# Performance work log

Measured on AMD Instinct MI355X. Metric: run time of the kernel, lower is better.

The kernel has to match this reference:

```python
import jax, jax.numpy as jnp
import numpy as np

MARGIN = 0.5
TIME_GAP = 10
EPS = 1e-8  # torch cosine_similarity eps


def setup_inputs() -> dict:
    key = jax.random.key(0)
    hidden_states = jax.random.normal(key, (16, 4096, 512), dtype=jnp.float32)
    return {"hidden_states": hidden_states}


def _sim_shift(h, n, k):
    # cosine similarity between time t and t+k for all valid t, all batches
    # h: [B, S, D], n: [B, S] precomputed norms -> returns [B, S-k]
    dots = jnp.sum(h[:, :-k] * h[:, k:], axis=-1)
    denom = jnp.maximum(n[:, :-k] * n[:, k:], EPS)
    return dots / denom


def reference(hidden_states):
    h = hidden_states
    B, S, D = h.shape
    n = jnp.sqrt(jnp.sum(h * h, axis=-1))  # [B, S], computed once

    # adjacent: sum_t mean_b(1 - sim(t, t+1)) / (S-1) == overall mean
    adjacent_loss = jnp.mean(1.0 - _sim_shift(h, n, 1))

    # distant: shifts k in [TIME_GAP, 2*TIME_GAP), t in [0, S-k)
    distant_total = jnp.zeros((), dtype=h.dtype)
    count = 0
    for k in range(TIME_GAP, min(S, 2 * TIME_GAP)):
        sim = _sim_shift(h, n, k)  # [B, S-k]
        # original sums mean-over-batch per (t,k) pair
        distant_total = distant_total + jnp.sum(jnp.mean(jax.nn.relu(MARGIN - sim), axis=0))
        count += S - k
    distant_loss = distant_total / count if count > 0 else jnp.zeros((), dtype=h.dtype)

    return adjacent_loss + distant_loss
```

## Files before the change

### kernel.cpp

```cpp
#include <hip/hip_runtime.h>
#include <math.h>

constexpr int B_ = 16;
constexpr int S_ = 4096;
constexpr int D_ = 512;
constexpr float MARGIN = 0.5f;
constexpr float EPS = 1e-8f;

constexpr int T_   = 32;
constexpr int ROWS = T_ + 19;
constexpr int RS   = D_ + 8;
constexpr int NBLK = B_ * (S_ / T_);

typedef __attribute__((ext_vector_type(8))) short short8;
typedef __attribute__((ext_vector_type(4))) float floatx4;

template <int CTRL>
__device__ __forceinline__ float dpp_add(float x) {
    int m = __builtin_amdgcn_update_dpp(0, __float_as_int(x), CTRL, 0xf, 0xf, true);
    return x + __int_as_float(m);
}
__device__ __forceinline__ float wave_sum63(float x) {
    x = dpp_add<0x111>(x);
    x = dpp_add<0x112>(x);
    x = dpp_add<0x114>(x);
    x = dpp_add<0x118>(x);
    x = dpp_add<0x142>(x);
    x = dpp_add<0x143>(x);
    return x;
}

__global__ __launch_bounds__(256) void tcl_partial(const float* __restrict__ h,
                                                   float* __restrict__ ws) {
    __shared__ unsigned short sm[ROWS * RS];
    __shared__ float norms[ROWS];
    __shared__ float bsum[4];

    const int tid = threadIdx.x;
    const int b   = blockIdx.x >> 7;
    const int t0  = (blockIdx.x & 127) * T_;
    const float* base = h + (size_t)b * S_ * D_;

#pragma unroll
    for (int it = 0; it < 26; ++it) {
        const int idx = tid + it * 256;
        if (idx < ROWS * 128) {
            const int r  = idx >> 7;
            const int c4 = idx & 127;
            const int t  = t0 + r;
            float4 v = make_float4(0.f, 0.f, 0.f, 0.f);
            if (t < S_) v = *(const float4*)(base + (size_t)t * D_ + c4 * 4);
            ushort4 u;
            u.x = (unsigned short)(__float_as_uint(v.x) >> 16);
            u.y = (unsigned short)(__float_as_uint(v.y) >> 16);
            u.z = (unsigned short)(__float_as_uint(v.z) >> 16);
            u.w = (unsigned short)(__float_as_uint(v.w) >> 16);
            *(ushort4*)&sm[r * RS + c4 * 4] = u;
        }
    }
    __syncthreads();

    const int lane = tid & 63;
    const int w    = tid >> 6;
    const int m16  = lane & 15;
    const int q    = lane >> 4;

    const int AOFF[8] = {0, 0, 0, 16, 16, 16, 32, 35};
    const int BOFF[8] = {0, 16, 32, 16, 32, 35, 32, 35};
    const int CLO[8]  = {0, 16, 32, 16, 32, 48, 32, 48};
    const int CHI[8]  = {15, 31, 47, 31, 47, 50, 47, 50};
    const int DIAG[8] = {1, 0, 0, 1, 0, 0, 1, 1};
    const int SIMS[8] = {1, 1, 1, 1, 1, 1, 0, 0};

    floatx4 acc[2];
#pragma unroll
    for (int jj = 0; jj < 2; ++jj) {
        const int J = w + jj * 4;
        const unsigned short* pa = &sm[(AOFF[J] + m16) * RS + q * 8];
        const unsigned short* pb = &sm[(BOFF[J] + m16) * RS + q * 8];
        floatx4 c = {0.f, 0.f, 0.f, 0.f};
#pragma unroll
        for (int kk = 0; kk < 16; ++kk) {
            short8 af = *(const short8*)(pa + kk * 32);
            short8 bf = *(const short8*)(pb + kk * 32);
            c = __builtin_amdgcn_mfma_f32_16x16x32_bf16(af, bf, c, 0, 0, 0);
        }
        acc[jj] = c;
    }

#pragma unroll
    for (int jj = 0; jj < 2; ++jj) {
        const int J = w + jj * 4;
        if (DIAG[J]) {
            const int gcol = BOFF[J] + m16;
#pragma unroll
            for (int r = 0; r < 4; ++r) {
                const int grow = AOFF[J] + q * 4 + r;
                if (grow == gcol && gcol >= CLO[J] && gcol <= CHI[J])
                    norms[grow] = sqrtf(acc[jj][r]);
            }
        }
    }
    __syncthreads();

    const float w1 = 1.0f / ((float)B_ * (float)(S_ - 1));
    const float w2 = 1.0f / ((float)B_ * (float)(10 * S_ - 145));
    float local = 0.f;
#pragma unroll
    for (int jj = 0; jj < 2; ++jj) {
        const int J = w + jj * 4;
        if (SIMS[J]) {
            const int gcol = BOFF[J] + m16;
            if (gcol >= CLO[J] && gcol <= CHI[J] && (t0 + gcol) < S_) {
                const float nb = norms[gcol];
#pragma unroll
                for (int r = 0; r < 4; ++r) {
                    const int grow = AOFF[J] + q * 4 + r;
                    const int k = gcol - grow;
                    if (k == 1 || (k >= 10 && k <= 19)) {
                        const float na  = norms[grow];
                        const float sim = acc[jj][r] / fmaxf(na * nb, EPS);
                        local += (k == 1) ? w1 * (1.0f - sim)
                                          : w2 * fmaxf(MARGIN - sim, 0.f);
                    }
                }
            }
        }
    }

    local = wave_sum63(local);
    if (lane == 63) bsum[w] = local;
    __syncthreads();
    if (tid == 0) ws[blockIdx.x] = bsum[0] + bsum[1] + bsum[2] + bsum[3];
}

__global__ __launch_bounds__(1024) void tcl_final(const float* __restrict__ ws,
                                                  float* __restrict__ out) {
    float v = 0.f;
    for (int j = threadIdx.x; j < NBLK; j += 1024) v += ws[j];
    v = wave_sum63(v);
    __shared__ float s[16];
    if ((threadIdx.x & 63) == 63) s[threadIdx.x >> 6] = v;
    __syncthreads();
    if (threadIdx.x == 0) {
        float t = 0.f;
#pragma unroll
        for (int j = 0; j < 16; j++) t += s[j];
        out[0] = t;
    }
}

extern "C" void kernel_launch(void* const* d_in, const int* in_sizes, int n_in,
                              void* d_out, int out_size, void* d_ws, size_t ws_size,
                              hipStream_t stream) {
    const float* h = (const float*)d_in[0];
    float* out = (float*)d_out;
    float* ws = (float*)d_ws;
    tcl_partial<<<NBLK, 256, 0, stream>>>(h, ws);
    tcl_final<<<1, 1024, 0, stream>>>(ws, out);
}
```

Measured before the change: 208.4 us.

## Shrink time tile to 8 and stage fp32 rows via direct global-to-LDS loads

```diff
diff --git a/kernel.cpp b/kernel.cpp
--- a/kernel.cpp
+++ b/kernel.cpp
@@ -7,9 +7,9 @@
 constexpr float MARGIN = 0.5f;
 constexpr float EPS = 1e-8f;
 
-constexpr int T_   = 32;
+constexpr int T_   = 8;
 constexpr int ROWS = T_ + 19;
-constexpr int RS   = D_ + 8;
+constexpr int RSF  = 520;
 constexpr int NBLK = B_ * (S_ / T_);
 
 typedef __attribute__((ext_vector_type(8))) short short8;
@@ -30,75 +30,83 @@
     return x;
 }
 
-__global__ __launch_bounds__(256) void tcl_partial(const float* __restrict__ h,
-                                                   float* __restrict__ ws) {
-    __shared__ unsigned short sm[ROWS * RS];
+__device__ __forceinline__ short8 ldsfrag(const float* p) {
+    float4 a = *(const float4*)p;
+    float4 b = *(const float4*)(p + 4);
+    short8 s;
+    s[0] = (short)(__float_as_uint(a.x) >> 16);
+    s[1] = (short)(__float_as_uint(a.y) >> 16);
+    s[2] = (short)(__float_as_uint(a.z) >> 16);
+    s[3] = (short)(__float_as_uint(a.w) >> 16);
+    s[4] = (short)(__float_as_uint(b.x) >> 16);
+    s[5] = (short)(__float_as_uint(b.y) >> 16);
+    s[6] = (short)(__float_as_uint(b.z) >> 16);
+    s[7] = (short)(__float_as_uint(b.w) >> 16);
+    return s;
+}
+
+__global__ __launch_bounds__(256, 2) void tcl_partial(const float* __restrict__ h,
+                                                      float* __restrict__ ws) {
+    __shared__ float smf[ROWS * RSF];
     __shared__ float norms[ROWS];
     __shared__ float bsum[4];
 
-    const int tid = threadIdx.x;
-    const int b   = blockIdx.x >> 7;
-    const int t0  = (blockIdx.x & 127) * T_;
+    const int tid  = threadIdx.x;
+    const int lane = tid & 63;
+    const int w    = tid >> 6;
+
+    const int p  = blockIdx.x;
+    const int L  = (p & 7) * 1024 + (p >> 3);
+    const int b  = L >> 9;
+    const int t0 = (L & 511) * T_;
     const float* base = h + (size_t)b * S_ * D_;
 
-#pragma unroll
-    for (int it = 0; it < 26; ++it) {
-        const int idx = tid + it * 256;
-        if (idx < ROWS * 128) {
-            const int r  = idx >> 7;
-            const int c4 = idx & 127;
-            const int t  = t0 + r;
-            float4 v = make_float4(0.f, 0.f, 0.f, 0.f);
-            if (t < S_) v = *(const float4*)(base + (size_t)t * D_ + c4 * 4);
-            ushort4 u;
-            u.x = (unsigned short)(__float_as_uint(v.x) >> 16);
-            u.y = (unsigned short)(__float_as_uint(v.y) >> 16);
-            u.z = (unsigned short)(__float_as_uint(v.z) >> 16);
-            u.w = (unsigned short)(__float_as_uint(v.w) >> 16);
-            *(ushort4*)&sm[r * RS + c4 * 4] = u;
+    for (int c = w; c < 2 * ROWS; c += 4) {
+        const int r    = c >> 1;
+        const int half = c & 1;
+        const int t    = t0 + r;
+        float* ldst = &smf[r * RSF + half * 256];
+        if (t < S_) {
+            const float* gsrc = base + (size_t)t * D_ + half * 256 + lane * 4;
+            __builtin_amdgcn_global_load_lds(
+                (__attribute__((address_space(1))) void*)(gsrc),
+                (__attribute__((address_space(3))) void*)(ldst),
+                16, 0, 0);
+        } else {
+            ((float4*)ldst)[lane] = make_float4(0.f, 0.f, 0.f, 0.f);
         }
     }
     __syncthreads();
 
-    const int lane = tid & 63;
-    const int w    = tid >> 6;
-    const int m16  = lane & 15;
-    const int q    = lane >> 4;
+    const int m16 = lane & 15;
+    const int q   = lane >> 4;
+    const int q8  = q * 8;
 
-    const int AOFF[8] = {0, 0, 0, 16, 16, 16, 32, 35};
-    const int BOFF[8] = {0, 16, 32, 16, 32, 35, 32, 35};
-    const int CLO[8]  = {0, 16, 32, 16, 32, 48, 32, 48};
-    const int CHI[8]  = {15, 31, 47, 31, 47, 50, 47, 50};
-    const int DIAG[8] = {1, 0, 0, 1, 0, 0, 1, 1};
-    const int SIMS[8] = {1, 1, 1, 1, 1, 1, 0, 0};
-
-    floatx4 acc[2];
-#pragma unroll
-    for (int jj = 0; jj < 2; ++jj) {
-        const int J = w + jj * 4;
-        const unsigned short* pa = &sm[(AOFF[J] + m16) * RS + q * 8];
-        const unsigned short* pb = &sm[(BOFF[J] + m16) * RS + q * 8];
-        floatx4 c = {0.f, 0.f, 0.f, 0.f};
+    const int AR[3] = {0, 0, 11};
+    const int BR[3] = {0, 11, 11};
+    floatx4 acc = {0.f, 0.f, 0.f, 0.f};
+    if (w < 3) {
+        const float* pa = &smf[(AR[w] + m16) * RSF + q8];
+        const float* pb = &smf[(BR[w] + m16) * RSF + q8];
 #pragma unroll
         for (int kk = 0; kk < 16; ++kk) {
-            short8 af = *(const short8*)(pa + kk * 32);
-            short8 bf = *(const short8*)(pb + kk * 32);
-            c = __builtin_amdgcn_mfma_f32_16x16x32_bf16(af, bf, c, 0, 0, 0);
+            short8 af = ldsfrag(pa + kk * 32);
+            short8 bf = ldsfrag(pb + kk * 32);
+            acc = __builtin_amdgcn_mfma_f32_16x16x32_bf16(af, bf, acc, 0, 0, 0);
         }
-        acc[jj] = c;
     }
 
+    if (w == 0) {
+        const int gcol = m16;
 #pragma unroll
-    for (int jj = 0; jj < 2; ++jj) {
-        const int J = w + jj * 4;
-        if (DIAG[J]) {
-            const int gcol = BOFF[J] + m16;
+        for (int r = 0; r < 4; ++r)
+            if (q * 4 + r == gcol) norms[gcol] = sqrtf(acc[r]);
+    } else if (w == 2) {
+        const int gcol = 11 + m16;
+        if (gcol >= 16) {
 #pragma unroll
-            for (int r = 0; r < 4; ++r) {
-                const int grow = AOFF[J] + q * 4 + r;
-                if (grow == gcol && gcol >= CLO[J] && gcol <= CHI[J])
-                    norms[grow] = sqrtf(acc[jj][r]);
-            }
+            for (int r = 0; r < 4; ++r)
+                if (11 + q * 4 + r == gcol) norms[gcol] = sqrtf(acc[r]);
         }
     }
     __syncthreads();
@@ -106,23 +114,32 @@
     const float w1 = 1.0f / ((float)B_ * (float)(S_ - 1));
     const float w2 = 1.0f / ((float)B_ * (float)(10 * S_ - 145));
     float local = 0.f;
+    if (w == 0) {
+        const int gcol = m16;
+        if (gcol <= 10 && (t0 + gcol) < S_) {
+            const float nb = norms[gcol];
 #pragma unroll
-    for (int jj = 0; jj < 2; ++jj) {
-        const int J = w + jj * 4;
-        if (SIMS[J]) {
-            const int gcol = BOFF[J] + m16;
-            if (gcol >= CLO[J] && gcol <= CHI[J] && (t0 + gcol) < S_) {
-                const float nb = norms[gcol];
+            for (int r = 0; r < 4; ++r) {
+                const int grow = q * 4 + r;
+                const int k = gcol - grow;
+                if (grow < T_ && (k == 1 || k == 10)) {
+                    const float sim = acc[r] / fmaxf(norms[grow] * nb, EPS);
+                    local += (k == 1) ? w1 * (1.0f - sim)
+                                      : w2 * fmaxf(MARGIN - sim, 0.f);
+                }
+            }
+        }
+    } else if (w == 1) {
+        const int gcol = 11 + m16;
+        if ((t0 + gcol) < S_) {
+            const float nb = norms[gcol];
 #pragma unroll
-                for (int r = 0; r < 4; ++r) {
-                    const int grow = AOFF[J] + q * 4 + r;
-                    const int k = gcol - grow;
-                    if (k == 1 || (k >= 10 && k <= 19)) {
-                        const float na  = norms[grow];
-                        const float sim = acc[jj][r] / fmaxf(na * nb, EPS);
-                        local += (k == 1) ? w1 * (1.0f - sim)
-                                          : w2 * fmaxf(MARGIN - sim, 0.f);
-                    }
+            for (int r = 0; r < 4; ++r) {
+                const int grow = q * 4 + r;
+                const int k = gcol - grow;
+                if (grow < T_ && k >= 10 && k <= 19) {
+                    const float sim = acc[r] / fmaxf(norms[grow] * nb, EPS);
+                    local += w2 * fmaxf(MARGIN - sim, 0.f);
                 }
             }
         }
```

Result: slower. 219.8 us (+5.5%).

## Load MFMA fragments directly from global per wave, dropping LDS staging

Applied to the files above, without the earlier changes.

```diff
diff --git a/kernel.cpp b/kernel.cpp
--- a/kernel.cpp
+++ b/kernel.cpp
@@ -7,10 +7,10 @@
 constexpr float MARGIN = 0.5f;
 constexpr float EPS = 1e-8f;
 
-constexpr int T_   = 32;
-constexpr int ROWS = T_ + 19;
-constexpr int RS   = D_ + 8;
-constexpr int NBLK = B_ * (S_ / T_);
+constexpr int TGR = 32;
+constexpr int WPB = 4;
+constexpr int NBLK = B_ * S_ / (TGR * WPB);
+constexpr int NW   = NBLK * WPB;
 
 typedef __attribute__((ext_vector_type(8))) short short8;
 typedef __attribute__((ext_vector_type(4))) float floatx4;
@@ -30,114 +30,105 @@
     return x;
 }
 
-__global__ __launch_bounds__(256) void tcl_partial(const float* __restrict__ h,
-                                                   float* __restrict__ ws) {
-    __shared__ unsigned short sm[ROWS * RS];
-    __shared__ float norms[ROWS];
-    __shared__ float bsum[4];
+__device__ __forceinline__ unsigned int pk(float lo, float hi) {
+    return (__float_as_uint(lo) >> 16) | (__float_as_uint(hi) & 0xffff0000u);
+}
 
-    const int tid = threadIdx.x;
-    const int b   = blockIdx.x >> 7;
-    const int t0  = (blockIdx.x & 127) * T_;
-    const float* base = h + (size_t)b * S_ * D_;
+__global__ __launch_bounds__(256, 2) void tcl_partial(const float* __restrict__ h,
+                                                      float* __restrict__ ws) {
+    __shared__ float nlds[WPB][64];
+
+    const int tid  = threadIdx.x;
+    const int lane = tid & 63;
+    const int w    = tid >> 6;
+
+    const int p  = blockIdx.x;
+    const int L  = (p & 7) * (NBLK / 8) + (p >> 3);
+    const int gw = L * WPB + w;
+    const int b  = gw >> 7;
+    const int t0 = (gw & 127) * TGR;
+
+    const int m16 = lane & 15;
+    const int q   = lane >> 4;
+    const int q8  = q * 8;
+
+    const float* fb[4];
+#pragma unroll
+    for (int o = 0; o < 4; ++o) {
+        int t = t0 + o * 16 + m16;
+        if (t > S_ - 1) t = S_ - 1;
+        fb[o] = h + ((size_t)b * S_ + t) * D_ + q8;
+    }
+
+    floatx4 acc[8];
+#pragma unroll
+    for (int j = 0; j < 8; ++j) acc[j] = (floatx4){0.f, 0.f, 0.f, 0.f};
 
 #pragma unroll
-    for (int it = 0; it < 26; ++it) {
-        const int idx = tid + it * 256;
-        if (idx < ROWS * 128) {
-            const int r  = idx >> 7;
-            const int c4 = idx & 127;
-            const int t  = t0 + r;
-            float4 v = make_float4(0.f, 0.f, 0.f, 0.f);
-            if (t < S_) v = *(const float4*)(base + (size_t)t * D_ + c4 * 4);
-            ushort4 u;
-            u.x = (unsigned short)(__float_as_uint(v.x) >> 16);
-            u.y = (unsigned short)(__float_as_uint(v.y) >> 16);
-            u.z = (unsigned short)(__float_as_uint(v.z) >> 16);
-            u.w = (unsigned short)(__float_as_uint(v.w) >> 16);
-            *(ushort4*)&sm[r * RS + c4 * 4] = u;
+    for (int kk = 0; kk < 16; ++kk) {
+        short8 f[4];
+#pragma unroll
+        for (int o = 0; o < 4; ++o) {
+            float4 x = *(const float4*)(fb[o] + kk * 32);
+            float4 y = *(const float4*)(fb[o] + kk * 32 + 4);
+            union { uint4 u4; short8 s8; } cv;
+            cv.u4.x = pk(x.x, x.y);
+            cv.u4.y = pk(x.z, x.w);
+            cv.u4.z = pk(y.x, y.y);
+            cv.u4.w = pk(y.z, y.w);
+            f[o] = cv.s8;
         }
-    }
-    __syncthreads();
-
-    const int lane = tid & 63;
-    const int w    = tid >> 6;
-    const int m16  = lane & 15;
-    const int q    = lane >> 4;
-
-    const int AOFF[8] = {0, 0, 0, 16, 16, 16, 32, 35};
-    const int BOFF[8] = {0, 16, 32, 16, 32, 35, 32, 35};
-    const int CLO[8]  = {0, 16, 32, 16, 32, 48, 32, 48};
-    const int CHI[8]  = {15, 31, 47, 31, 47, 50, 47, 50};
-    const int DIAG[8] = {1, 0, 0, 1, 0, 0, 1, 1};
-    const int SIMS[8] = {1, 1, 1, 1, 1, 1, 0, 0};
-
-    floatx4 acc[2];
-#pragma unroll
-    for (int jj = 0; jj < 2; ++jj) {
-        const int J = w + jj * 4;
-        const unsigned short* pa = &sm[(AOFF[J] + m16) * RS + q * 8];
-        const unsigned short* pb = &sm[(BOFF[J] + m16) * RS + q * 8];
-        floatx4 c = {0.f, 0.f, 0.f, 0.f};
-#pragma unroll
-        for (int kk = 0; kk < 16; ++kk) {
-            short8 af = *(const short8*)(pa + kk * 32);
-            short8 bf = *(const short8*)(pb + kk * 32);
-            c = __builtin_amdgcn_mfma_f32_16x16x32_bf16(af, bf, c, 0, 0, 0);
-        }
-        acc[jj] = c;
+        acc[0] = __builtin_amdgcn_mfma_f32_16x16x32_bf16(f[0], f[0], acc[0], 0, 0, 0);
+        acc[1] = __builtin_amdgcn_mfma_f32_16x16x32_bf16(f[0], f[1], acc[1], 0, 0, 0);
+        acc[2] = __builtin_amdgcn_mfma_f32_16x16x32_bf16(f[0], f[2], acc[2], 0, 0, 0);
+        acc[3] = __builtin_amdgcn_mfma_f32_16x16x32_bf16(f[1], f[1], acc[3], 0, 0, 0);
+        acc[4] = __builtin_amdgcn_mfma_f32_16x16x32_bf16(f[1], f[2], acc[4], 0, 0, 0);
+        acc[5] = __builtin_amdgcn_mfma_f32_16x16x32_bf16(f[1], f[3], acc[5], 0, 0, 0);
+        acc[6] = __builtin_amdgcn_mfma_f32_16x16x32_bf16(f[2], f[2], acc[6], 0, 0, 0);
+        acc[7] = __builtin_amdgcn_mfma_f32_16x16x32_bf16(f[3], f[3], acc[7], 0, 0, 0);
     }
 
+    const int DJ[4] = {0, 3, 6, 7};
+    const int DB[4] = {0, 16, 32, 48};
 #pragma unroll
-    for (int jj = 0; jj < 2; ++jj) {
-        const int J = w + jj * 4;
-        if (DIAG[J]) {
-            const int gcol = BOFF[J] + m16;
+    for (int d = 0; d < 4; ++d) {
 #pragma unroll
-            for (int r = 0; r < 4; ++r) {
-                const int grow = AOFF[J] + q * 4 + r;
-                if (grow == gcol && gcol >= CLO[J] && gcol <= CHI[J])
-                    norms[grow] = sqrtf(acc[jj][r]);
-            }
-        }
+        for (int r = 0; r < 4; ++r)
+            if (q * 4 + r == m16) nlds[w][DB[d] + m16] = sqrtf(acc[DJ[d]][r]);
     }
     __syncthreads();
 
     const float w1 = 1.0f / ((float)B_ * (float)(S_ - 1));
     const float w2 = 1.0f / ((float)B_ * (float)(10 * S_ - 145));
+    const int SA[6] = {0, 0, 0, 16, 16, 16};
+    const int SB[6] = {0, 16, 32, 16, 32, 48};
     float local = 0.f;
 #pragma unroll
-    for (int jj = 0; jj < 2; ++jj) {
-        const int J = w + jj * 4;
-        if (SIMS[J]) {
-            const int gcol = BOFF[J] + m16;
-            if (gcol >= CLO[J] && gcol <= CHI[J] && (t0 + gcol) < S_) {
-                const float nb = norms[gcol];
+    for (int s2 = 0; s2 < 6; ++s2) {
+        const int gcol = SB[s2] + m16;
+        if (t0 + gcol < S_) {
+            const float nb = nlds[w][gcol];
 #pragma unroll
-                for (int r = 0; r < 4; ++r) {
-                    const int grow = AOFF[J] + q * 4 + r;
-                    const int k = gcol - grow;
-                    if (k == 1 || (k >= 10 && k <= 19)) {
-                        const float na  = norms[grow];
-                        const float sim = acc[jj][r] / fmaxf(na * nb, EPS);
-                        local += (k == 1) ? w1 * (1.0f - sim)
-                                          : w2 * fmaxf(MARGIN - sim, 0.f);
-                    }
+            for (int r = 0; r < 4; ++r) {
+                const int grow = SA[s2] + q * 4 + r;
+                const int k = gcol - grow;
+                if (k == 1 || (k >= 10 && k <= 19)) {
+                    const float sim = acc[s2][r] / fmaxf(nlds[w][grow] * nb, EPS);
+                    local += (k == 1) ? w1 * (1.0f - sim)
+                                      : w2 * fmaxf(MARGIN - sim, 0.f);
                 }
             }
         }
     }
 
     local = wave_sum63(local);
-    if (lane == 63) bsum[w] = local;
-    __syncthreads();
-    if (tid == 0) ws[blockIdx.x] = bsum[0] + bsum[1] + bsum[2] + bsum[3];
+    if (lane == 63) ws[gw] = local;
 }
 
 __global__ __launch_bounds__(1024) void tcl_final(const float* __restrict__ ws,
                                                   float* __restrict__ out) {
     float v = 0.f;
-    for (int j = threadIdx.x; j < NBLK; j += 1024) v += ws[j];
+    for (int j = threadIdx.x; j < NW; j += 1024) v += ws[j];
     v = wave_sum63(v);
     __shared__ float s[16];
     if ((threadIdx.x & 63) == 63) s[threadIdx.x >> 6] = v;
```

After: 202.1 us. -3.1%, faster.
